# Kernel tuning notes

Hardware: AMD Instinct MI355X
Metric: run time of the kernel (lower is better)

## Reference

```python
import jax, jax.numpy as jnp
import numpy as np

N = 4096        # n_locations
D_MODEL = 512
H, D_K, D_V = 4, 128, 256


def setup_inputs() -> dict:
    key = jax.random.key(0)
    ks = jax.random.split(key, 7)
    s = 0.02
    return {
        "Q": jax.random.normal(ks[0], (N, D_MODEL), dtype=jnp.float32),
        "K": jax.random.normal(ks[1], (N, D_MODEL), dtype=jnp.float32),
        "V": jax.random.normal(ks[2], (N, D_MODEL), dtype=jnp.float32),
        "Wq": jax.random.normal(ks[3], (H, D_MODEL, D_K), dtype=jnp.float32) * s,
        "Wk": jax.random.normal(ks[4], (H, D_MODEL, D_K), dtype=jnp.float32) * s,
        "Wv": jax.random.normal(ks[5], (H, D_MODEL, D_V), dtype=jnp.float32) * s,
        "Wo": jax.random.normal(ks[6], (D_MODEL, H * D_V), dtype=jnp.float32) * s,
    }


def reference(Q, K, V, Wq, Wk, Wv, Wo):
    n = K.shape[0]
    # Batched per-head projections: [h, n, d_k] / [h, n, d_v]
    q = jnp.einsum('nd,hdk->hnk', Q, Wq)
    k = jnp.einsum('nd,hdk->hnk', K, Wk)
    v = jnp.einsum('nd,hdv->hnv', V, Wv)
    # NOTE: original scales by sqrt(n_locations) (K.size(0)), not sqrt(d_k)
    scores = jnp.einsum('hqk,hnk->hqn', q, k) / jnp.sqrt(jnp.asarray(n, q.dtype))
    weights = jax.nn.softmax(scores, axis=-1)          # [h, n, n]
    heads = jnp.einsum('hqn,hnv->hqv', weights, v)      # [h, n, d_v]
    # concat heads along feature dim: [n, h*d_v]
    x = jnp.transpose(heads, (1, 0, 2)).reshape(heads.shape[1], -1)
    return x @ Wo.T                                     # [n, d_model]
```

## Files before the change

### kernel.cpp

```cpp
#include <hip/hip_runtime.h>
#include <hip/hip_bf16.h>
#include <type_traits>

typedef __hip_bfloat16 bf16;
typedef __attribute__((ext_vector_type(8))) short bf16x8;
typedef __attribute__((ext_vector_type(4))) float f32x4;

#define N_LOC 4096
#define DMODEL 512
#define NHEAD 4
#define DK 128
#define DV 256

__device__ __forceinline__ bf16 to_bf16(float f) { return __float2bfloat16(f); }

__device__ __forceinline__ void dma16(const bf16* g, bf16* l) {
  __builtin_amdgcn_global_load_lds((const __attribute__((address_space(1))) unsigned int*)g,
                                   (__attribute__((address_space(3))) unsigned int*)l, 16, 0, 0);
}

__global__ __launch_bounds__(256) void convert_all(const float* __restrict__ Q,
                                                   const float* __restrict__ K,
                                                   const float* __restrict__ V,
                                                   const float* __restrict__ Wo,
                                                   bf16* __restrict__ Qb, bf16* __restrict__ Kb,
                                                   bf16* __restrict__ Vb, bf16* __restrict__ Wob) {
  long i = ((long)blockIdx.x * 256 + threadIdx.x) * 8;
  const float* src;
  bf16* dst;
  long off;
  if (i < 2097152)      { src = Q;  dst = Qb;  off = i; }
  else if (i < 4194304) { src = K;  dst = Kb;  off = i - 2097152; }
  else if (i < 6291456) { src = V;  dst = Vb;  off = i - 4194304; }
  else                  { src = Wo; dst = Wob; off = i - 6291456; }
  float4 a = *(const float4*)&src[off];
  float4 b = *(const float4*)&src[off + 4];
  union { bf16 h[8]; bf16x8 v; } u;
  u.h[0] = to_bf16(a.x); u.h[1] = to_bf16(a.y); u.h[2] = to_bf16(a.z); u.h[3] = to_bf16(a.w);
  u.h[4] = to_bf16(b.x); u.h[5] = to_bf16(b.y); u.h[6] = to_bf16(b.z); u.h[7] = to_bf16(b.w);
  *(bf16x8*)&dst[off] = u.v;
}

__global__ __launch_bounds__(256) void pack_wt(const float* __restrict__ Wq,
                                               const float* __restrict__ Wk,
                                               const float* __restrict__ Wv,
                                               bf16* __restrict__ oq, bf16* __restrict__ ok,
                                               bf16* __restrict__ ov) {
  int z = blockIdx.z;
  const float* W = (z == 0) ? Wq : (z == 1) ? Wk : Wv;
  bf16* out = (z == 0) ? oq : (z == 1) ? ok : ov;
  int DH = (z == 2) ? 256 : 128;
  int nt = DH >> 6;
  int y = blockIdx.y;
  if (y >= 4 * nt) return;
  int h = y / nt, tt = y - h * nt;
  int d0 = blockIdx.x * 64, t0 = tt * 64;
  __shared__ float tile[64][65];
  for (int i = threadIdx.x; i < 4096; i += 256) {
    int r = i >> 6, c = i & 63;
    tile[r][c] = W[((size_t)h * 512 + d0 + r) * DH + t0 + c];
  }
  __syncthreads();
  for (int i = threadIdx.x; i < 4096; i += 256) {
    int t = i >> 6, d = i & 63;
    out[((size_t)(h * DH + t0 + t)) * 512 + d0 + d] = to_bf16(tile[d][t]);
  }
}

template <typename OutT>
__global__ __launch_bounds__(256) void gemm_bt(const bf16* __restrict__ A,
                                               const bf16* __restrict__ Bt,
                                               OutT* __restrict__ C, int M, int N, int K) {
  const int LD = 72;
  __shared__ bf16 As[64 * LD];
  __shared__ bf16 Bs[64 * LD];
  int tid = threadIdx.x;
  int lane = tid & 63, w = tid >> 6;
  int quad = lane >> 4, l16 = lane & 15;
  int wm = (w >> 1) * 32, wn = (w & 1) * 32;
  int m0 = blockIdx.x * 64, n0 = blockIdx.y * 64;

  f32x4 acc[2][2] = {};
  for (int k0 = 0; k0 < K; k0 += 64) {
    for (int i = tid; i < 64 * 8; i += 256) {
      int r = i >> 3, c = (i & 7) * 8;
      *(bf16x8*)&As[r * LD + c] = *(const bf16x8*)&A[(long)(m0 + r) * K + k0 + c];
      *(bf16x8*)&Bs[r * LD + c] = *(const bf16x8*)&Bt[(long)(n0 + r) * K + k0 + c];
    }
    __syncthreads();
#pragma unroll
    for (int kk = 0; kk < 2; kk++) {
      bf16x8 af[2], bfr[2];
#pragma unroll
      for (int i = 0; i < 2; i++)
        af[i] = *(const bf16x8*)&As[(wm + i * 16 + l16) * LD + kk * 32 + quad * 8];
#pragma unroll
      for (int j = 0; j < 2; j++)
        bfr[j] = *(const bf16x8*)&Bs[(wn + j * 16 + l16) * LD + kk * 32 + quad * 8];
#pragma unroll
      for (int i = 0; i < 2; i++)
#pragma unroll
        for (int j = 0; j < 2; j++)
          acc[i][j] = __builtin_amdgcn_mfma_f32_16x16x32_bf16(af[i], bfr[j], acc[i][j], 0, 0, 0);
    }
    __syncthreads();
  }
#pragma unroll
  for (int i = 0; i < 2; i++)
#pragma unroll
    for (int j = 0; j < 2; j++)
#pragma unroll
      for (int r = 0; r < 4; r++) {
        long row = m0 + wm + i * 16 + quad * 4 + r;
        long col = n0 + wn + j * 16 + l16;
        if constexpr (std::is_same<OutT, bf16>::value)
          C[row * N + col] = to_bf16(acc[i][j][r]);
        else
          C[row * N + col] = acc[i][j][r];
      }
}

__global__ __launch_bounds__(256) void transpose_bf16(const bf16* __restrict__ in,
                                                      bf16* __restrict__ out, int R, int Cc) {
  __shared__ bf16 t[64][65];
  int r0 = blockIdx.x * 64, c0 = blockIdx.y * 64;
  for (int i = threadIdx.x; i < 64 * 64; i += 256) {
    int r = i >> 6, c = i & 63;
    t[r][c] = in[(long)(r0 + r) * Cc + c0 + c];
  }
  __syncthreads();
  for (int i = threadIdx.x; i < 64 * 64; i += 256) {
    int c = i >> 6, r = i & 63;
    out[(long)(c0 + c) * R + r0 + r] = t[r][c];
  }
}

__global__ __launch_bounds__(512, 4) void attn(const bf16* __restrict__ qb,
                                               const bf16* __restrict__ kb,
                                               const bf16* __restrict__ vT,
                                               bf16* __restrict__ x) {
  __shared__ __align__(16) bf16 kt[64 * 128];
  __shared__ __align__(16) bf16 vt[256 * 64];
  __shared__ __align__(16) bf16 pt[64 * 72];
  __shared__ float Lrow[64];

  const int head = blockIdx.x & 3;
  const int q0 = (blockIdx.x >> 2) * 64;
  const int tid = threadIdx.x;
  const int lane = tid & 63, w = tid >> 6;
  const int quad = lane >> 4, l16 = lane & 15;
  const int cd = w & 3;
  const int g = w >> 2;

  bf16x8 onesf;
  {
    union { bf16 h[8]; bf16x8 v; } u;
    bf16 one = to_bf16(1.0f), zero = to_bf16(0.0f);
#pragma unroll
    for (int j = 0; j < 8; j++) u.h[j] = (l16 == 0) ? one : zero;
    onesf = u.v;
  }

  bf16x8 qf[2][4];
#pragma unroll
  for (int i = 0; i < 2; i++) {
    const bf16* qrow = &qb[(size_t)(q0 + g * 32 + i * 16 + l16) * 512 + head * 128];
#pragma unroll
    for (int kk = 0; kk < 4; kk++) qf[i][kk] = *(const bf16x8*)&qrow[kk * 32 + quad * 8];
  }

  f32x4 oacc[2][4] = {};
  f32x4 oL[2] = {};
  const float scale = 1.0f / 64.0f;

  for (int key0 = 0; key0 < N_LOC; key0 += 64) {
#pragma unroll
    for (int t2 = 0; t2 < 2; t2++) {
      int j = 2 * w + t2;
      int r = 4 * j + (lane >> 4);
      int p = lane & 15;
      int G = (p & 8) | ((p ^ r) & 7);
      dma16(&kb[(size_t)(key0 + r) * 512 + head * 128 + G * 8], &kt[j * 512]);
    }
#pragma unroll
    for (int t2 = 0; t2 < 4; t2++) {
      int j = 4 * w + t2;
      int r = 8 * j + (lane >> 3);
      int p = lane & 7;
      int G = (p ^ r) & 7;
      dma16(&vT[(size_t)(head * 256 + r) * 4096 + key0 + G * 8], &vt[j * 512]);
    }
    __syncthreads();

    f32x4 sacc[2] = {};
#pragma unroll
    for (int kk = 0; kk < 4; kk++) {
      int R = cd * 16 + l16;
      int G = kk * 4 + quad;
      bf16x8 kf = *(const bf16x8*)&kt[R * 128 + (((G ^ R) & 7) | (G & 8)) * 8];
      sacc[0] = __builtin_amdgcn_mfma_f32_16x16x32_bf16(qf[0][kk], kf, sacc[0], 0, 0, 0);
      sacc[1] = __builtin_amdgcn_mfma_f32_16x16x32_bf16(qf[1][kk], kf, sacc[1], 0, 0, 0);
    }
#pragma unroll
    for (int i = 0; i < 2; i++)
#pragma unroll
      for (int r = 0; r < 4; r++)
        pt[(g * 32 + i * 16 + quad * 4 + r) * 72 + cd * 16 + l16] =
            to_bf16(__expf(sacc[i][r] * scale));
    __syncthreads();

#pragma unroll
    for (int kk = 0; kk < 2; kk++) {
      bf16x8 pf[2];
#pragma unroll
      for (int i = 0; i < 2; i++)
        pf[i] = *(const bf16x8*)&pt[(g * 32 + i * 16 + l16) * 72 + kk * 32 + quad * 8];
#pragma unroll
      for (int c = 0; c < 4; c++) {
        int R = cd * 64 + c * 16 + l16;
        int G = kk * 4 + quad;
        bf16x8 vf = *(const bf16x8*)&vt[R * 64 + ((G ^ R) & 7) * 8];
#pragma unroll
        for (int i = 0; i < 2; i++)
          oacc[i][c] = __builtin_amdgcn_mfma_f32_16x16x32_bf16(pf[i], vf, oacc[i][c], 0, 0, 0);
      }
      if (cd == 3) {
#pragma unroll
        for (int i = 0; i < 2; i++)
          oL[i] = __builtin_amdgcn_mfma_f32_16x16x32_bf16(pf[i], onesf, oL[i], 0, 0, 0);
      }
    }
    __syncthreads();
  }

  if (cd == 3 && l16 == 0) {
#pragma unroll
    for (int i = 0; i < 2; i++)
#pragma unroll
      for (int r = 0; r < 4; r++) Lrow[g * 32 + i * 16 + quad * 4 + r] = oL[i][r];
  }
  __syncthreads();

#pragma unroll
  for (int i = 0; i < 2; i++)
#pragma unroll
    for (int c = 0; c < 4; c++)
#pragma unroll
      for (int r = 0; r < 4; r++) {
        int row = g * 32 + i * 16 + quad * 4 + r;
        float v = oacc[i][c][r] / Lrow[row];
        x[(size_t)(q0 + row) * 1024 + head * 256 + cd * 64 + c * 16 + l16] = to_bf16(v);
      }
}

extern "C" void kernel_launch(void* const* d_in, const int* in_sizes, int n_in,
                              void* d_out, int out_size, void* d_ws, size_t ws_size,
                              hipStream_t stream) {
  const float* Q  = (const float*)d_in[0];
  const float* Km = (const float*)d_in[1];
  const float* V  = (const float*)d_in[2];
  const float* Wq = (const float*)d_in[3];
  const float* Wk = (const float*)d_in[4];
  const float* Wv = (const float*)d_in[5];
  const float* Wo = (const float*)d_in[6];
  float* out = (float*)d_out;

  bf16* ws  = (bf16*)d_ws;
  bf16* Qb  = ws;
  bf16* Kb  = Qb + 2097152;
  bf16* Vb  = Kb + 2097152;
  bf16* Wqt = Vb + 2097152;
  bf16* Wkt = Wqt + 262144;
  bf16* Wvt = Wkt + 262144;
  bf16* Wob = Wvt + 524288;
  bf16* qb  = Wob + 524288;
  bf16* kb  = qb + 2097152;
  bf16* vb  = kb + 2097152;
  bf16* vT  = vb + 4194304;
  bf16* x   = vT + 4194304;

  convert_all<<<3328, 256, 0, stream>>>(Q, Km, V, Wo, Qb, Kb, Vb, Wob);
  pack_wt<<<dim3(8, 16, 3), 256, 0, stream>>>(Wq, Wk, Wv, Wqt, Wkt, Wvt);

  gemm_bt<bf16><<<dim3(64, 8), 256, 0, stream>>>(Qb, Wqt, qb, 4096, 512, 512);
  gemm_bt<bf16><<<dim3(64, 8), 256, 0, stream>>>(Kb, Wkt, kb, 4096, 512, 512);
  gemm_bt<bf16><<<dim3(64, 16), 256, 0, stream>>>(Vb, Wvt, vb, 4096, 1024, 512);
  transpose_bf16<<<dim3(64, 16), 256, 0, stream>>>(vb, vT, 4096, 1024);

  attn<<<256, 512, 0, stream>>>(qb, kb, vT, x);

  gemm_bt<float><<<dim3(64, 8), 256, 0, stream>>>(x, Wob, out, 4096, 512, 1024);
}
```

Baseline: 249.4 us.

## Merge prep/projection launches, fuse V transpose, retile attention to 256 threads

Merges the convert and weight-pack kernels into one launch, and the three projection GEMMs into one launch. The V projection now writes its transposed output directly through shared memory, which removes the separate transpose kernel and the intermediate vb buffer. The attention kernel goes from 8 to 4 waves per block, so each wave computes a 64x64 output slab with more accumulators and more MFMA reuse of the P fragments. This trades fewer launches and less traffic for higher register pressure and fewer waves per CU during attention.

```diff
diff --git a/kernel.cpp b/kernel.cpp
--- a/kernel.cpp
+++ b/kernel.cpp
@@ -1,16 +1,11 @@
 #include <hip/hip_runtime.h>
 #include <hip/hip_bf16.h>
-#include <type_traits>
 
 typedef __hip_bfloat16 bf16;
 typedef __attribute__((ext_vector_type(8))) short bf16x8;
 typedef __attribute__((ext_vector_type(4))) float f32x4;
 
 #define N_LOC 4096
-#define DMODEL 512
-#define NHEAD 4
-#define DK 128
-#define DV 256
 
 __device__ __forceinline__ bf16 to_bf16(float f) { return __float2bfloat16(f); }
 
@@ -19,42 +14,40 @@
                                    (__attribute__((address_space(3))) unsigned int*)l, 16, 0, 0);
 }
 
-__global__ __launch_bounds__(256) void convert_all(const float* __restrict__ Q,
-                                                   const float* __restrict__ K,
-                                                   const float* __restrict__ V,
-                                                   const float* __restrict__ Wo,
-                                                   bf16* __restrict__ Qb, bf16* __restrict__ Kb,
-                                                   bf16* __restrict__ Vb, bf16* __restrict__ Wob) {
-  long i = ((long)blockIdx.x * 256 + threadIdx.x) * 8;
-  const float* src;
-  bf16* dst;
-  long off;
-  if (i < 2097152)      { src = Q;  dst = Qb;  off = i; }
-  else if (i < 4194304) { src = K;  dst = Kb;  off = i - 2097152; }
-  else if (i < 6291456) { src = V;  dst = Vb;  off = i - 4194304; }
-  else                  { src = Wo; dst = Wob; off = i - 6291456; }
-  float4 a = *(const float4*)&src[off];
-  float4 b = *(const float4*)&src[off + 4];
-  union { bf16 h[8]; bf16x8 v; } u;
-  u.h[0] = to_bf16(a.x); u.h[1] = to_bf16(a.y); u.h[2] = to_bf16(a.z); u.h[3] = to_bf16(a.w);
-  u.h[4] = to_bf16(b.x); u.h[5] = to_bf16(b.y); u.h[6] = to_bf16(b.z); u.h[7] = to_bf16(b.w);
-  *(bf16x8*)&dst[off] = u.v;
-}
-
-__global__ __launch_bounds__(256) void pack_wt(const float* __restrict__ Wq,
-                                               const float* __restrict__ Wk,
-                                               const float* __restrict__ Wv,
-                                               bf16* __restrict__ oq, bf16* __restrict__ ok,
-                                               bf16* __restrict__ ov) {
-  int z = blockIdx.z;
+__global__ __launch_bounds__(256) void prep(const float* __restrict__ Q, const float* __restrict__ K,
+                                            const float* __restrict__ V, const float* __restrict__ Wo,
+                                            const float* __restrict__ Wq, const float* __restrict__ Wk,
+                                            const float* __restrict__ Wv,
+                                            bf16* __restrict__ Qb, bf16* __restrict__ Kb,
+                                            bf16* __restrict__ Vb, bf16* __restrict__ Wob,
+                                            bf16* __restrict__ oq, bf16* __restrict__ ok,
+                                            bf16* __restrict__ ov) {
+  int b = blockIdx.x;
+  if (b < 3328) {
+    long i = ((long)b * 256 + threadIdx.x) * 8;
+    const float* src; bf16* dst; long off;
+    if (i < 2097152)      { src = Q;  dst = Qb;  off = i; }
+    else if (i < 4194304) { src = K;  dst = Kb;  off = i - 2097152; }
+    else if (i < 6291456) { src = V;  dst = Vb;  off = i - 4194304; }
+    else                  { src = Wo; dst = Wob; off = i - 6291456; }
+    float4 a = *(const float4*)&src[off];
+    float4 c = *(const float4*)&src[off + 4];
+    union { bf16 h[8]; bf16x8 v; } u;
+    u.h[0] = to_bf16(a.x); u.h[1] = to_bf16(a.y); u.h[2] = to_bf16(a.z); u.h[3] = to_bf16(a.w);
+    u.h[4] = to_bf16(c.x); u.h[5] = to_bf16(c.y); u.h[6] = to_bf16(c.z); u.h[7] = to_bf16(c.w);
+    *(bf16x8*)&dst[off] = u.v;
+    return;
+  }
+  int t = b - 3328;
+  int z = t >> 7, rem = t & 127;
+  int xb = rem & 7, y = rem >> 3;
   const float* W = (z == 0) ? Wq : (z == 1) ? Wk : Wv;
   bf16* out = (z == 0) ? oq : (z == 1) ? ok : ov;
   int DH = (z == 2) ? 256 : 128;
   int nt = DH >> 6;
-  int y = blockIdx.y;
   if (y >= 4 * nt) return;
   int h = y / nt, tt = y - h * nt;
-  int d0 = blockIdx.x * 64, t0 = tt * 64;
+  int d0 = xb * 64, t0 = tt * 64;
   __shared__ float tile[64][65];
   for (int i = threadIdx.x; i < 4096; i += 256) {
     int r = i >> 6, c = i & 63;
@@ -62,15 +55,203 @@
   }
   __syncthreads();
   for (int i = threadIdx.x; i < 4096; i += 256) {
-    int t = i >> 6, d = i & 63;
-    out[((size_t)(h * DH + t0 + t)) * 512 + d0 + d] = to_bf16(tile[d][t]);
-  }
-}
-
-template <typename OutT>
-__global__ __launch_bounds__(256) void gemm_bt(const bf16* __restrict__ A,
-                                               const bf16* __restrict__ Bt,
-                                               OutT* __restrict__ C, int M, int N, int K) {
+    int tr = i >> 6, d = i & 63;
+    out[((size_t)(h * DH + t0 + tr)) * 512 + d0 + d] = to_bf16(tile[d][tr]);
+  }
+}
+
+__global__ __launch_bounds__(256) void proj_gemm(const bf16* __restrict__ Qb, const bf16* __restrict__ Wqt,
+                                                 const bf16* __restrict__ Kb, const bf16* __restrict__ Wkt,
+                                                 const bf16* __restrict__ Vb, const bf16* __restrict__ Wvt,
+                                                 bf16* __restrict__ qb, bf16* __restrict__ kb,
+                                                 bf16* __restrict__ vT) {
+  const int LD = 72;
+  __shared__ bf16 As[64 * LD];
+  __shared__ bf16 Bs[64 * LD];
+  int b = blockIdx.x;
+  const bf16 *A, *Bt;
+  bf16* Cout;
+  int N, m0, n0, tr;
+  if (b < 512)       { A = Qb; Bt = Wqt; Cout = qb; N = 512;  m0 = (b >> 3) * 64; n0 = (b & 7) * 64;  tr = 0; }
+  else if (b < 1024) { b -= 512;  A = Kb; Bt = Wkt; Cout = kb; N = 512;  m0 = (b >> 3) * 64; n0 = (b & 7) * 64;  tr = 0; }
+  else               { b -= 1024; A = Vb; Bt = Wvt; Cout = vT; N = 1024; m0 = (b >> 4) * 64; n0 = (b & 15) * 64; tr = 1; }
+
+  int tid = threadIdx.x;
+  int lane = tid & 63, w = tid >> 6;
+  int quad = lane >> 4, l16 = lane & 15;
+  int wm = (w >> 1) * 32, wn = (w & 1) * 32;
+
+  f32x4 acc[2][2] = {};
+  for (int k0 = 0; k0 < 512; k0 += 64) {
+    for (int i = tid; i < 64 * 8; i += 256) {
+      int r = i >> 3, c = (i & 7) * 8;
+      *(bf16x8*)&As[r * LD + c] = *(const bf16x8*)&A[(size_t)(m0 + r) * 512 + k0 + c];
+      *(bf16x8*)&Bs[r * LD + c] = *(const bf16x8*)&Bt[(size_t)(n0 + r) * 512 + k0 + c];
+    }
+    __syncthreads();
+#pragma unroll
+    for (int kk = 0; kk < 2; kk++) {
+      bf16x8 af[2], bfr[2];
+#pragma unroll
+      for (int i = 0; i < 2; i++)
+        af[i] = *(const bf16x8*)&As[(wm + i * 16 + l16) * LD + kk * 32 + quad * 8];
+#pragma unroll
+      for (int j = 0; j < 2; j++)
+        bfr[j] = *(const bf16x8*)&Bs[(wn + j * 16 + l16) * LD + kk * 32 + quad * 8];
+#pragma unroll
+      for (int i = 0; i < 2; i++)
+#pragma unroll
+        for (int j = 0; j < 2; j++)
+          acc[i][j] = __builtin_amdgcn_mfma_f32_16x16x32_bf16(af[i], bfr[j], acc[i][j], 0, 0, 0);
+    }
+    __syncthreads();
+  }
+  if (!tr) {
+#pragma unroll
+    for (int i = 0; i < 2; i++)
+#pragma unroll
+      for (int j = 0; j < 2; j++)
+#pragma unroll
+        for (int r = 0; r < 4; r++)
+          Cout[(size_t)(m0 + wm + i * 16 + quad * 4 + r) * N + n0 + wn + j * 16 + l16] =
+              to_bf16(acc[i][j][r]);
+  } else {
+    bf16* tb = As;
+#pragma unroll
+    for (int i = 0; i < 2; i++)
+#pragma unroll
+      for (int j = 0; j < 2; j++)
+#pragma unroll
+        for (int r = 0; r < 4; r++)
+          tb[(wn + j * 16 + l16) * LD + wm + i * 16 + quad * 4 + r] = to_bf16(acc[i][j][r]);
+    __syncthreads();
+    for (int idx = tid; idx < 512; idx += 256) {
+      int c = idx >> 3, s = idx & 7;
+      *(bf16x8*)&vT[(size_t)(n0 + c) * 4096 + m0 + s * 8] = *(const bf16x8*)&tb[c * LD + s * 8];
+    }
+  }
+}
+
+__global__ __launch_bounds__(256, 2) void attn(const bf16* __restrict__ qb,
+                                               const bf16* __restrict__ kb,
+                                               const bf16* __restrict__ vT,
+                                               bf16* __restrict__ x) {
+  __shared__ __align__(16) bf16 kt[64 * 128];
+  __shared__ __align__(16) bf16 vt[256 * 64];
+  __shared__ __align__(16) bf16 pt[64 * 72];
+  __shared__ float Lrow[64];
+
+  const int head = blockIdx.x & 3;
+  const int q0 = (blockIdx.x >> 2) * 64;
+  const int tid = threadIdx.x;
+  const int lane = tid & 63, w = tid >> 6;
+  const int quad = lane >> 4, l16 = lane & 15;
+  const int qh = w & 1, kh = w >> 1;
+
+  bf16x8 onesf;
+  {
+    union { bf16 h[8]; bf16x8 v; } u;
+    bf16 one = to_bf16(1.0f), zero = to_bf16(0.0f);
+#pragma unroll
+    for (int j = 0; j < 8; j++) u.h[j] = (l16 == 0) ? one : zero;
+    onesf = u.v;
+  }
+
+  bf16x8 qf[2][4];
+#pragma unroll
+  for (int i = 0; i < 2; i++) {
+    const bf16* qrow = &qb[(size_t)(q0 + qh * 32 + i * 16 + l16) * 512 + head * 128];
+#pragma unroll
+    for (int kk = 0; kk < 4; kk++) qf[i][kk] = *(const bf16x8*)&qrow[kk * 32 + quad * 8];
+  }
+
+  f32x4 oacc[4][4] = {};
+  f32x4 oL = {};
+  const float scale = 1.0f / 64.0f;
+
+  for (int key0 = 0; key0 < N_LOC; key0 += 64) {
+#pragma unroll
+    for (int t = 0; t < 4; t++) {
+      int j = 4 * w + t;
+      int r = 4 * j + (lane >> 4);
+      int p = lane & 15;
+      int G = (p & 8) | ((p ^ r) & 7);
+      dma16(&kb[(size_t)(key0 + r) * 512 + head * 128 + G * 8], &kt[j * 512]);
+    }
+#pragma unroll
+    for (int t = 0; t < 8; t++) {
+      int j = 8 * w + t;
+      int r = 8 * j + (lane >> 3);
+      int p = lane & 7;
+      int G = (p ^ r) & 7;
+      dma16(&vT[(size_t)(head * 256 + r) * 4096 + key0 + G * 8], &vt[j * 512]);
+    }
+    __syncthreads();
+
+    f32x4 sacc[2][2] = {};
+#pragma unroll
+    for (int kk = 0; kk < 4; kk++) {
+#pragma unroll
+      for (int t = 0; t < 2; t++) {
+        int R = kh * 32 + t * 16 + l16;
+        int G = kk * 4 + quad;
+        bf16x8 kf = *(const bf16x8*)&kt[R * 128 + (((G ^ R) & 7) | (G & 8)) * 8];
+#pragma unroll
+        for (int i = 0; i < 2; i++)
+          sacc[i][t] = __builtin_amdgcn_mfma_f32_16x16x32_bf16(qf[i][kk], kf, sacc[i][t], 0, 0, 0);
+      }
+    }
+#pragma unroll
+    for (int i = 0; i < 2; i++)
+#pragma unroll
+      for (int t = 0; t < 2; t++)
+#pragma unroll
+        for (int r = 0; r < 4; r++)
+          pt[(qh * 32 + i * 16 + quad * 4 + r) * 72 + kh * 32 + t * 16 + l16] =
+              to_bf16(__expf(sacc[i][t][r] * scale));
+    __syncthreads();
+
+#pragma unroll
+    for (int kk = 0; kk < 2; kk++) {
+      bf16x8 pf[4];
+#pragma unroll
+      for (int i = 0; i < 4; i++)
+        pf[i] = *(const bf16x8*)&pt[(i * 16 + l16) * 72 + kk * 32 + quad * 8];
+      oL = __builtin_amdgcn_mfma_f32_16x16x32_bf16(pf[w], onesf, oL, 0, 0, 0);
+#pragma unroll
+      for (int c = 0; c < 4; c++) {
+        int R = w * 64 + c * 16 + l16;
+        int G = kk * 4 + quad;
+        bf16x8 vf = *(const bf16x8*)&vt[R * 64 + ((G ^ R) & 7) * 8];
+#pragma unroll
+        for (int i = 0; i < 4; i++)
+          oacc[i][c] = __builtin_amdgcn_mfma_f32_16x16x32_bf16(pf[i], vf, oacc[i][c], 0, 0, 0);
+      }
+    }
+    __syncthreads();
+  }
+
+  if (l16 == 0) {
+#pragma unroll
+    for (int r = 0; r < 4; r++) Lrow[w * 16 + quad * 4 + r] = oL[r];
+  }
+  __syncthreads();
+
+#pragma unroll
+  for (int i = 0; i < 4; i++)
+#pragma unroll
+    for (int c = 0; c < 4; c++)
+#pragma unroll
+      for (int r = 0; r < 4; r++) {
+        int row = i * 16 + quad * 4 + r;
+        float v = oacc[i][c][r] / Lrow[row];
+        x[(size_t)(q0 + row) * 1024 + head * 256 + w * 64 + c * 16 + l16] = to_bf16(v);
+      }
+}
+
+__global__ __launch_bounds__(256) void out_gemm(const bf16* __restrict__ A,
+                                                const bf16* __restrict__ Bt,
+                                                float* __restrict__ C) {
   const int LD = 72;
   __shared__ bf16 As[64 * LD];
   __shared__ bf16 Bs[64 * LD];
@@ -81,11 +262,11 @@
   int m0 = blockIdx.x * 64, n0 = blockIdx.y * 64;
 
   f32x4 acc[2][2] = {};
-  for (int k0 = 0; k0 < K; k0 += 64) {
+  for (int k0 = 0; k0 < 1024; k0 += 64) {
     for (int i = tid; i < 64 * 8; i += 256) {
       int r = i >> 3, c = (i & 7) * 8;
-      *(bf16x8*)&As[r * LD + c] = *(const bf16x8*)&A[(long)(m0 + r) * K + k0 + c];
-      *(bf16x8*)&Bs[r * LD + c] = *(const bf16x8*)&Bt[(long)(n0 + r) * K + k0 + c];
+      *(bf16x8*)&As[r * LD + c] = *(const bf16x8*)&A[(size_t)(m0 + r) * 1024 + k0 + c];
+      *(bf16x8*)&Bs[r * LD + c] = *(const bf16x8*)&Bt[(size_t)(n0 + r) * 1024 + k0 + c];
     }
     __syncthreads();
 #pragma unroll
@@ -110,147 +291,9 @@
 #pragma unroll
     for (int j = 0; j < 2; j++)
 #pragma unroll
-      for (int r = 0; r < 4; r++) {
-        long row = m0 + wm + i * 16 + quad * 4 + r;
-        long col = n0 + wn + j * 16 + l16;
-        if constexpr (std::is_same<OutT, bf16>::value)
-          C[row * N + col] = to_bf16(acc[i][j][r]);
-        else
-          C[row * N + col] = acc[i][j][r];
-      }
-}
-
-__global__ __launch_bounds__(256) void transpose_bf16(const bf16* __restrict__ in,
-                                                      bf16* __restrict__ out, int R, int Cc) {
-  __shared__ bf16 t[64][65];
-  int r0 = blockIdx.x * 64, c0 = blockIdx.y * 64;
-  for (int i = threadIdx.x; i < 64 * 64; i += 256) {
-    int r = i >> 6, c = i & 63;
-    t[r][c] = in[(long)(r0 + r) * Cc + c0 + c];
-  }
-  __syncthreads();
-  for (int i = threadIdx.x; i < 64 * 64; i += 256) {
-    int c = i >> 6, r = i & 63;
-    out[(long)(c0 + c) * R + r0 + r] = t[r][c];
-  }
-}
-
-__global__ __launch_bounds__(512, 4) void attn(const bf16* __restrict__ qb,
-                                               const bf16* __restrict__ kb,
-                                               const bf16* __restrict__ vT,
-                                               bf16* __restrict__ x) {
-  __shared__ __align__(16) bf16 kt[64 * 128];
-  __shared__ __align__(16) bf16 vt[256 * 64];
-  __shared__ __align__(16) bf16 pt[64 * 72];
-  __shared__ float Lrow[64];
-
-  const int head = blockIdx.x & 3;
-  const int q0 = (blockIdx.x >> 2) * 64;
-  const int tid = threadIdx.x;
-  const int lane = tid & 63, w = tid >> 6;
-  const int quad = lane >> 4, l16 = lane & 15;
-  const int cd = w & 3;
-  const int g = w >> 2;
-
-  bf16x8 onesf;
-  {
-    union { bf16 h[8]; bf16x8 v; } u;
-    bf16 one = to_bf16(1.0f), zero = to_bf16(0.0f);
-#pragma unroll
-    for (int j = 0; j < 8; j++) u.h[j] = (l16 == 0) ? one : zero;
-    onesf = u.v;
-  }
-
-  bf16x8 qf[2][4];
-#pragma unroll
-  for (int i = 0; i < 2; i++) {
-    const bf16* qrow = &qb[(size_t)(q0 + g * 32 + i * 16 + l16) * 512 + head * 128];
-#pragma unroll
-    for (int kk = 0; kk < 4; kk++) qf[i][kk] = *(const bf16x8*)&qrow[kk * 32 + quad * 8];
-  }
-
-  f32x4 oacc[2][4] = {};
-  f32x4 oL[2] = {};
-  const float scale = 1.0f / 64.0f;
-
-  for (int key0 = 0; key0 < N_LOC; key0 += 64) {
-#pragma unroll
-    for (int t2 = 0; t2 < 2; t2++) {
-      int j = 2 * w + t2;
-      int r = 4 * j + (lane >> 4);
-      int p = lane & 15;
-      int G = (p & 8) | ((p ^ r) & 7);
-      dma16(&kb[(size_t)(key0 + r) * 512 + head * 128 + G * 8], &kt[j * 512]);
-    }
-#pragma unroll
-    for (int t2 = 0; t2 < 4; t2++) {
-      int j = 4 * w + t2;
-      int r = 8 * j + (lane >> 3);
-      int p = lane & 7;
-      int G = (p ^ r) & 7;
-      dma16(&vT[(size_t)(head * 256 + r) * 4096 + key0 + G * 8], &vt[j * 512]);
-    }
-    __syncthreads();
-
-    f32x4 sacc[2] = {};
-#pragma unroll
-    for (int kk = 0; kk < 4; kk++) {
-      int R = cd * 16 + l16;
-      int G = kk * 4 + quad;
-      bf16x8 kf = *(const bf16x8*)&kt[R * 128 + (((G ^ R) & 7) | (G & 8)) * 8];
-      sacc[0] = __builtin_amdgcn_mfma_f32_16x16x32_bf16(qf[0][kk], kf, sacc[0], 0, 0, 0);
-      sacc[1] = __builtin_amdgcn_mfma_f32_16x16x32_bf16(qf[1][kk], kf, sacc[1], 0, 0, 0);
-    }
-#pragma unroll
-    for (int i = 0; i < 2; i++)
-#pragma unroll
       for (int r = 0; r < 4; r++)
-        pt[(g * 32 + i * 16 + quad * 4 + r) * 72 + cd * 16 + l16] =
-            to_bf16(__expf(sacc[i][r] * scale));
-    __syncthreads();
-
-#pragma unroll
-    for (int kk = 0; kk < 2; kk++) {
-      bf16x8 pf[2];
-#pragma unroll
-      for (int i = 0; i < 2; i++)
-        pf[i] = *(const bf16x8*)&pt[(g * 32 + i * 16 + l16) * 72 + kk * 32 + quad * 8];
-#pragma unroll
-      for (int c = 0; c < 4; c++) {
-        int R = cd * 64 + c * 16 + l16;
-        int G = kk * 4 + quad;
-        bf16x8 vf = *(const bf16x8*)&vt[R * 64 + ((G ^ R) & 7) * 8];
-#pragma unroll
-        for (int i = 0; i < 2; i++)
-          oacc[i][c] = __builtin_amdgcn_mfma_f32_16x16x32_bf16(pf[i], vf, oacc[i][c], 0, 0, 0);
-      }
-      if (cd == 3) {
-#pragma unroll
-        for (int i = 0; i < 2; i++)
-          oL[i] = __builtin_amdgcn_mfma_f32_16x16x32_bf16(pf[i], onesf, oL[i], 0, 0, 0);
-      }
-    }
-    __syncthreads();
-  }
-
-  if (cd == 3 && l16 == 0) {
-#pragma unroll
-    for (int i = 0; i < 2; i++)
-#pragma unroll
-      for (int r = 0; r < 4; r++) Lrow[g * 32 + i * 16 + quad * 4 + r] = oL[i][r];
-  }
-  __syncthreads();
-
-#pragma unroll
-  for (int i = 0; i < 2; i++)
-#pragma unroll
-    for (int c = 0; c < 4; c++)
-#pragma unroll
-      for (int r = 0; r < 4; r++) {
-        int row = g * 32 + i * 16 + quad * 4 + r;
-        float v = oacc[i][c][r] / Lrow[row];
-        x[(size_t)(q0 + row) * 1024 + head * 256 + cd * 64 + c * 16 + l16] = to_bf16(v);
-      }
+        C[(size_t)(m0 + wm + i * 16 + quad * 4 + r) * 512 + n0 + wn + j * 16 + l16] =
+            acc[i][j][r];
 }
 
 extern "C" void kernel_launch(void* const* d_in, const int* in_sizes, int n_in,
@@ -275,19 +318,11 @@
   bf16* Wob = Wvt + 524288;
   bf16* qb  = Wob + 524288;
   bf16* kb  = qb + 2097152;
-  bf16* vb  = kb + 2097152;
-  bf16* vT  = vb + 4194304;
+  bf16* vT  = kb + 2097152;
   bf16* x   = vT + 4194304;
 
-  convert_all<<<3328, 256, 0, stream>>>(Q, Km, V, Wo, Qb, Kb, Vb, Wob);
-  pack_wt<<<dim3(8, 16, 3), 256, 0, stream>>>(Wq, Wk, Wv, Wqt, Wkt, Wvt);
-
-  gemm_bt<bf16><<<dim3(64, 8), 256, 0, stream>>>(Qb, Wqt, qb, 4096, 512, 512);
-  gemm_bt<bf16><<<dim3(64, 8), 256, 0, stream>>>(Kb, Wkt, kb, 4096, 512, 512);
-  gemm_bt<bf16><<<dim3(64, 16), 256, 0, stream>>>(Vb, Wvt, vb, 4096, 1024, 512);
-  transpose_bf16<<<dim3(64, 16), 256, 0, stream>>>(vb, vT, 4096, 1024);
-
-  attn<<<256, 512, 0, stream>>>(qb, kb, vT, x);
-
-  gemm_bt<float><<<dim3(64, 8), 256, 0, stream>>>(x, Wob, out, 4096, 512, 1024);
-}
+  prep<<<3712, 256, 0, stream>>>(Q, Km, V, Wo, Wq, Wk, Wv, Qb, Kb, Vb, Wob, Wqt, Wkt, Wvt);
+  proj_gemm<<<2048, 256, 0, stream>>>(Qb, Wqt, Kb, Wkt, Vb, Wvt, qb, kb, vT);
+  attn<<<256, 256, 0, stream>>>(qb, kb, vT, x);
+  out_gemm<<<dim3(64, 8), 256, 0, stream>>>(x, Wob, out);
+}
```

New measurement: 324.0 us. 29.9% more time.
